# Optimization experiments

Hardware: AMD Instinct MI355X
Metric: run time of the kernel (lower is better)

Reference implementation:

```python
import jax, jax.numpy as jnp
import numpy as np

NHEADS = 16
HEAD_DIM = 128
HIDDEN = 2048
SOFTCAP = 50.0
ROPE_BASE = 10000.0
SCALE = 256.0 ** (-0.5)  # hardcoded in original, NOT head_dim**-0.5


def _rope_tables(T, D, dtype):
    inv_freq = 1.0 / (ROPE_BASE ** (jnp.arange(0, D, 2, dtype=jnp.float32) / D))
    pos = jnp.arange(T, dtype=jnp.float32)
    freqs = pos[:, None] * inv_freq[None, :]            # [T, D/2]
    emb = jnp.concatenate([freqs, freqs], axis=-1)      # [T, D]
    # broadcast shape [1, 1, T, D] for (B, H, T, D) q/k
    return jnp.cos(emb)[None, None].astype(dtype), jnp.sin(emb)[None, None].astype(dtype)


def _rotate_half(x):
    x1, x2 = x[..., : x.shape[-1] // 2], x[..., x.shape[-1] // 2:]
    return jnp.concatenate([-x2, x1], axis=-1)


def setup_inputs() -> dict:
    key = jax.random.key(0)
    ks = jax.random.split(key, 5)
    B, T = 1, 4096
    X = jax.random.normal(ks[0], (B, T, HIDDEN), dtype=jnp.float32)
    std = 0.02
    Wq = jax.random.normal(ks[1], (HIDDEN, NHEADS * HEAD_DIM), dtype=jnp.float32) * std
    Wk = jax.random.normal(ks[2], (HIDDEN, NHEADS * HEAD_DIM), dtype=jnp.float32) * std
    Wv = jax.random.normal(ks[3], (HIDDEN, NHEADS * HEAD_DIM), dtype=jnp.float32) * std
    Wo = jax.random.normal(ks[4], (NHEADS * HEAD_DIM, HIDDEN), dtype=jnp.float32) * std
    return {"X": X, "Wq": Wq, "Wk": Wk, "Wv": Wv, "Wo": Wo}


def reference(X, Wq, Wk, Wv, Wo):
    B, T, C = X.shape
    H, D = NHEADS, HEAD_DIM
    # QKV projections -> [B, H, T, D]
    q = (X @ Wq).reshape(B, T, H, D).transpose(0, 2, 1, 3)
    k = (X @ Wk).reshape(B, T, H, D).transpose(0, 2, 1, 3)
    v = (X @ Wv).reshape(B, T, H, D).transpose(0, 2, 1, 3)
    # RoPE
    cos, sin = _rope_tables(T, D, X.dtype)
    q = q * cos + _rotate_half(q) * sin
    k = k * cos + _rotate_half(k) * sin
    # attention logits with tanh softcapping
    att = jnp.einsum("bhqd,bhkd->bhqk", q, k) * SCALE
    att = jnp.tanh(att / SOFTCAP) * SOFTCAP
    causal = jnp.tril(jnp.ones((T, T), dtype=bool))[None, None]
    att = jnp.where(causal, att, -jnp.inf)
    att = jax.nn.softmax(att, axis=-1)
    # dropout is identity (train=False)
    y = jnp.einsum("bhqk,bhkd->bhqd", att, v)
    y = y.transpose(0, 2, 1, 3).reshape(B, T, H * D)
    return y @ Wo
```

## Files before the change

kernel.cpp:

```cpp
#include <hip/hip_runtime.h>
#include <stdint.h>

#define T_SEQ 4096
#define HID   2048
#define NH    16
#define HD    128

typedef __attribute__((ext_vector_type(8))) short short8;
typedef __attribute__((ext_vector_type(4))) short short4v;
typedef __attribute__((ext_vector_type(4))) float f32x4;

typedef __attribute__((address_space(1))) void as1_void;
typedef __attribute__((address_space(3))) void as3_void;

__device__ __forceinline__ unsigned short f2bf(float f){
  unsigned u = __builtin_bit_cast(unsigned, f);
  u += 0x7fffu + ((u >> 16) & 1u);
  return (unsigned short)(u >> 16);
}
__device__ __forceinline__ float bf2f(unsigned short b){
  unsigned u = ((unsigned)b) << 16;
  return __builtin_bit_cast(float, u);
}
__device__ __forceinline__ void gll16(const void* g, void* l){
  __builtin_amdgcn_global_load_lds((as1_void*)(uintptr_t)g,
                                   (as3_void*)(unsigned)(uintptr_t)l, 16, 0, 0);
}

__global__ __launch_bounds__(256) void conv_x_k(const float* __restrict__ X,
                                                unsigned short* __restrict__ O){
  int i = (blockIdx.x * 256 + threadIdx.x) * 4;
  float4 v = *(const float4*)(X + i);
  short4v o;
  o[0] = (short)f2bf(v.x); o[1] = (short)f2bf(v.y);
  o[2] = (short)f2bf(v.z); o[3] = (short)f2bf(v.w);
  *(short4v*)(O + i) = o;
}

__global__ __launch_bounds__(256) void conv_wt_k(const float* __restrict__ W0,
                                                 const float* __restrict__ W1,
                                                 const float* __restrict__ W2,
                                                 const float* __restrict__ W3,
                                                 unsigned short* __restrict__ Wt){
  const float* W = (blockIdx.z == 0) ? W0 : (blockIdx.z == 1) ? W1
                   : (blockIdx.z == 2) ? W2 : W3;
  unsigned short* out = Wt + (size_t)blockIdx.z * HID * HID;
  __shared__ float tile[32][33];
  const int x = threadIdx.x;
  const int y = threadIdx.y;
  const int k0 = blockIdx.y * 32, n0 = blockIdx.x * 32;
#pragma unroll
  for (int i = 0; i < 4; ++i){
    int r = y * 4 + i;
    tile[r][x] = W[(size_t)(k0 + r) * HID + n0 + x];
  }
  __syncthreads();
#pragma unroll
  for (int i = 0; i < 4; ++i){
    int r = y * 4 + i;
    out[(size_t)(n0 + r) * HID + k0 + x] = f2bf(tile[x][r]);
  }
}

template<int MODE, int NTOT>
__global__ __launch_bounds__(256, 3) void gemm_bt(
    const unsigned short* __restrict__ A,
    const unsigned short* __restrict__ Bt,
    unsigned short* __restrict__ Qb,
    unsigned short* __restrict__ Kb,
    unsigned short* __restrict__ Vt,
    float* __restrict__ Cf)
{
  constexpr int K = HID;
  __shared__ __align__(16) unsigned short lA[128 * 64];
  __shared__ __align__(16) unsigned short lB[128 * 64];

  const int tid  = threadIdx.x;
  const int wave = tid >> 6;
  const int lane = tid & 63;
  const int qd   = lane >> 4;
  const int mm   = lane & 15;
  const int m7   = mm & 7;
  const int wm   = wave >> 1;
  const int wn   = wave & 1;
  const int bm   = blockIdx.y * 128;
  const int bn   = blockIdx.x * 128;

  const unsigned short* ga[4];
  const unsigned short* gb[4];
  unsigned short* la[4];
  unsigned short* lbp[4];
#pragma unroll
  for (int i = 0; i < 4; ++i){
    int s0   = (wave * 4 + i) * 64;
    int slot = s0 + lane;
    int row  = slot >> 3;
    int kb   = (slot & 7) ^ (row & 7);
    ga[i]  = A  + (size_t)(bm + row) * K + kb * 8;
    gb[i]  = Bt + (size_t)(bn + row) * K + kb * 8;
    la[i]  = lA + s0 * 8;
    lbp[i] = lB + s0 * 8;
  }

  int abase[4], bbase[4];
#pragma unroll
  for (int t = 0; t < 4; ++t){
    abase[t] = (wm * 64 + t * 16 + mm) * 8;
    bbase[t] = (wn * 64 + t * 16 + mm) * 8;
  }

  const f32x4 fzero = {0.f, 0.f, 0.f, 0.f};
  f32x4 acc[4][4];
#pragma unroll
  for (int i = 0; i < 4; ++i)
#pragma unroll
    for (int j = 0; j < 4; ++j) acc[i][j] = fzero;

  for (int k0 = 0; k0 < K; k0 += 64){
    __syncthreads();
#pragma unroll
    for (int i = 0; i < 4; ++i){
      gll16(ga[i] + k0, la[i]);
      gll16(gb[i] + k0, lbp[i]);
    }
    __syncthreads();
#pragma unroll
    for (int ks = 0; ks < 2; ++ks){
      const int co = (ks * 4 + qd) ^ m7;
      short8 af[4], bfv[4];
#pragma unroll
      for (int t = 0; t < 4; ++t) af[t]  = *(const short8*)(lA + (abase[t] + co) * 8);
#pragma unroll
      for (int t = 0; t < 4; ++t) bfv[t] = *(const short8*)(lB + (bbase[t] + co) * 8);
#pragma unroll
      for (int i = 0; i < 4; ++i)
#pragma unroll
        for (int j = 0; j < 4; ++j)
          acc[i][j] = __builtin_amdgcn_mfma_f32_16x16x32_bf16(af[i], bfv[j], acc[i][j], 0, 0, 0);
    }
  }

#pragma unroll
  for (int i = 0; i < 4; ++i){
#pragma unroll
    for (int j = 0; j < 4; ++j){
      const int col = bn + wn * 64 + j * 16 + mm;
#pragma unroll
      for (int r = 0; r < 4; ++r){
        const int row = bm + wm * 64 + i * 16 + qd * 4 + r;
        const float v = acc[i][j][r];
        if (MODE == 0){
          const int sel = col >> 11;
          const int nn  = col & 2047;
          const int h   = nn >> 7;
          const int d   = nn & 127;
          const unsigned short bv = f2bf(v);
          if (sel == 0)      Qb[((size_t)h * T_SEQ + row) * HD + d] = bv;
          else if (sel == 1) Kb[((size_t)h * T_SEQ + row) * HD + d] = bv;
          else               Vt[((size_t)(h * HD + d)) * T_SEQ + row] = bv;
        } else {
          Cf[(size_t)row * NTOT + col] = v;
        }
      }
    }
  }
}

__global__ __launch_bounds__(256) void rope_k(unsigned short* __restrict__ Qb,
                                              unsigned short* __restrict__ Kb){
  const int j = threadIdx.x & 63;
  const int t = blockIdx.x * 4 + (threadIdx.x >> 6);
  const int h = blockIdx.y;
  const float fr = (float)t * __expf(-(float)j * (9.210340371976184f / 64.f));
  const float cs = cosf(fr), sn = sinf(fr);
  const size_t base = ((size_t)h * T_SEQ + t) * HD;
  {
    float x1 = bf2f(Qb[base + j]), x2 = bf2f(Qb[base + j + 64]);
    Qb[base + j]      = f2bf(x1 * cs - x2 * sn);
    Qb[base + j + 64] = f2bf(x2 * cs + x1 * sn);
  }
  {
    float x1 = bf2f(Kb[base + j]), x2 = bf2f(Kb[base + j + 64]);
    Kb[base + j]      = f2bf(x1 * cs - x2 * sn);
    Kb[base + j + 64] = f2bf(x2 * cs + x1 * sn);
  }
}

__global__ __launch_bounds__(256, 2) void attn_k(
    const unsigned short* __restrict__ Qb,
    const unsigned short* __restrict__ Kb,
    const unsigned short* __restrict__ Vt,
    unsigned short* __restrict__ Yb)
{
  __shared__ __align__(16) unsigned char smem[41216];
  unsigned short* lK = (unsigned short*)smem;
  unsigned short* lV = (unsigned short*)(smem + 16384);
  unsigned short (*lP)[32][32] = (unsigned short(*)[32][32])(smem + 32768);
  float* lL = (float*)(smem + 40960);
  float* lO = (float*)smem;

  const int tid  = threadIdx.x;
  const int w    = tid >> 6;
  const int rg   = w >> 1;
  const int kg   = w & 1;
  const int lane = tid & 63;
  const int qd   = lane >> 4;
  const int cc   = lane & 15;
  const int cx   = cc & 7;
  const int r8   = lane >> 3, c7 = lane & 7;

  const int b = blockIdx.x;
  const int h = (b & 7) + 8 * (b >> 8);
  const int pairP = (b >> 3) & 31;

  const int ce  = cc ^ qd;
  const int dlt = (ce & 4) ? -32 : 32;
  const unsigned short* gKbp = Kb + ((size_t)h * T_SEQ + w * 16 + qd) * HD + ce * 8;
  const int cV = c7 ^ r8;
  const unsigned short* gVbp = Vt + ((size_t)h * HD + w * 32 + r8) * T_SEQ + cV * 8;

  const f32x4 fzero = {0.f, 0.f, 0.f, 0.f};
  const float A0 = 0.0625f;
  const float A1 = -3.2552083e-8f;
  const float A2 = 2.0345052e-14f;

#pragma unroll 1
  for (int half = 0; half < 2; ++half){
    const int tp = half ? (63 - pairP) : pairP;
    const int qrow0 = tp * 64 + rg * 32;
    const int iters = tp + 1;

    short8 qf[2][4];
#pragma unroll
    for (int mt = 0; mt < 2; ++mt)
#pragma unroll
      for (int ks = 0; ks < 4; ++ks)
        qf[mt][ks] = *(const short8*)(Qb + ((size_t)h * T_SEQ + qrow0 + mt * 16 + cc) * HD + ks * 32 + qd * 8);

    f32x4 o[2][8];
    float lsum[2][4];
#pragma unroll
    for (int mt = 0; mt < 2; ++mt){
#pragma unroll
      for (int dn = 0; dn < 8; ++dn) o[mt][dn] = fzero;
#pragma unroll
      for (int r = 0; r < 4; ++r) lsum[mt][r] = 0.f;
    }

#pragma unroll 1
    for (int it = 0; it < iters; ++it){
      const int k0 = it * 64;
      __syncthreads();
      {
        const unsigned short* gK = gKbp + (size_t)k0 * HD;
        const unsigned short* gV = gVbp + k0;
        unsigned short* dK = lK + w * 2048;
        unsigned short* dV = lV + w * 2048;
#pragma unroll
        for (int i = 0; i < 4; ++i)
          gll16(gK + (size_t)(i * 4) * HD + ((i & 1) ? dlt : 0), dK + i * 512);
#pragma unroll
        for (int i = 0; i < 4; ++i)
          gll16(gV + (size_t)i * 8 * T_SEQ, dV + i * 512);
      }
      __syncthreads();

      f32x4 S[2][2];
#pragma unroll
      for (int mt = 0; mt < 2; ++mt)
#pragma unroll
        for (int nt = 0; nt < 2; ++nt) S[mt][nt] = fzero;
#pragma unroll
      for (int nt = 0; nt < 2; ++nt){
        short8 kf[4];
#pragma unroll
        for (int ks = 0; ks < 4; ++ks)
          kf[ks] = *(const short8*)(lK + ((kg * 32 + nt * 16 + cc) * 16 + ((ks * 4 + qd) ^ cx)) * 8);
#pragma unroll
        for (int mt = 0; mt < 2; ++mt)
#pragma unroll
          for (int ks = 0; ks < 4; ++ks)
            S[mt][nt] = __builtin_amdgcn_mfma_f32_16x16x32_bf16(qf[mt][ks], kf[ks], S[mt][nt], 0, 0, 0);
      }

      const bool domask = (it == iters - 1);
#pragma unroll
      for (int mt = 0; mt < 2; ++mt)
#pragma unroll
        for (int nt = 0; nt < 2; ++nt)
#pragma unroll
          for (int r = 0; r < 4; ++r){
            float s = S[mt][nt][r];
            float w2 = s * s;
            float t = fmaf(w2, A2, A1);
            t = fmaf(w2, t, A0);
            float a = s * t;
            a = fminf(fmaxf(a, -50.f), 50.f);
            float p = __expf(a);
            if (domask){
              int col = k0 + kg * 32 + nt * 16 + cc;
              int row = qrow0 + mt * 16 + qd * 4 + r;
              if (col > row) p = 0.f;
            }
            unsigned u = __builtin_bit_cast(unsigned, p);
            float pt = __builtin_bit_cast(float, u & 0xffff0000u);
            lsum[mt][r] += pt;
            lP[w][mt * 16 + qd * 4 + r][nt * 16 + cc] = (unsigned short)(u >> 16);
          }

      short8 pf[2];
#pragma unroll
      for (int mt = 0; mt < 2; ++mt)
        pf[mt] = *(const short8*)(&lP[w][mt * 16 + cc][qd * 8]);

#pragma unroll
      for (int dn = 0; dn < 8; ++dn){
        short8 vf = *(const short8*)(lV + ((dn * 16 + cc) * 8 + ((kg * 4 + qd) ^ cx)) * 8);
#pragma unroll
        for (int mt = 0; mt < 2; ++mt)
          o[mt][dn] = __builtin_amdgcn_mfma_f32_16x16x32_bf16(pf[mt], vf, o[mt][dn], 0, 0, 0);
      }
    }

    float lred[2][4];
#pragma unroll
    for (int mt = 0; mt < 2; ++mt)
#pragma unroll
      for (int r = 0; r < 4; ++r){
        float lb = lsum[mt][r];
        lb += __shfl_xor(lb, 1);
        lb += __shfl_xor(lb, 2);
        lb += __shfl_xor(lb, 4);
        lb += __shfl_xor(lb, 8);
        lred[mt][r] = lb;
      }

    __syncthreads();
    if (kg == 1){
#pragma unroll
      for (int mt = 0; mt < 2; ++mt){
#pragma unroll
        for (int dn = 0; dn < 8; ++dn)
          *(f32x4*)&lO[(dn * 16 + cc) * 68 + rg * 32 + mt * 16 + qd * 4] = o[mt][dn];
        if (cc == 0){
#pragma unroll
          for (int r = 0; r < 4; ++r)
            lL[rg * 32 + mt * 16 + qd * 4 + r] = lred[mt][r];
        }
      }
    }
    __syncthreads();
    if (kg == 0){
#pragma unroll
      for (int mt = 0; mt < 2; ++mt){
        float inv[4];
#pragma unroll
        for (int r = 0; r < 4; ++r){
          float lt = lred[mt][r] + lL[rg * 32 + mt * 16 + qd * 4 + r];
          inv[r] = __builtin_amdgcn_rcpf(lt);
        }
#pragma unroll
        for (int dn = 0; dn < 8; ++dn){
          f32x4 oo = o[mt][dn] + *(const f32x4*)&lO[(dn * 16 + cc) * 68 + rg * 32 + mt * 16 + qd * 4];
#pragma unroll
          for (int r = 0; r < 4; ++r){
            int row = qrow0 + mt * 16 + qd * 4 + r;
            Yb[(size_t)row * HID + h * HD + dn * 16 + cc] = f2bf(oo[r] * inv[r]);
          }
        }
      }
    }
    __syncthreads();
  }
}

extern "C" void kernel_launch(void* const* d_in, const int* in_sizes, int n_in,
                              void* d_out, int out_size, void* d_ws, size_t ws_size,
                              hipStream_t stream) {
  const float* X  = (const float*)d_in[0];
  const float* Wq = (const float*)d_in[1];
  const float* Wk = (const float*)d_in[2];
  const float* Wv = (const float*)d_in[3];
  const float* Wo = (const float*)d_in[4];
  float* out = (float*)d_out;

  unsigned short* ws = (unsigned short*)d_ws;
  unsigned short* Xb = ws;
  unsigned short* Wt = ws + (size_t)8  * 1024 * 1024;
  unsigned short* Qb = ws + (size_t)24 * 1024 * 1024;
  unsigned short* Kb = ws + (size_t)32 * 1024 * 1024;
  unsigned short* Vt = ws + (size_t)40 * 1024 * 1024;
  unsigned short* Yb = Xb;

  conv_x_k<<<8192, 256, 0, stream>>>(X, Xb);
  conv_wt_k<<<dim3(64, 64, 4), dim3(32, 8), 0, stream>>>(Wq, Wk, Wv, Wo, Wt);
  gemm_bt<0, 6144><<<dim3(48, 32), 256, 0, stream>>>(Xb, Wt, Qb, Kb, Vt, nullptr);
  rope_k<<<dim3(1024, NH), 256, 0, stream>>>(Qb, Kb);
  attn_k<<<dim3(512), 256, 0, stream>>>(Qb, Kb, Vt, Yb);
  gemm_bt<1, 2048><<<dim3(16, 32), 256, 0, stream>>>(Yb, Wt + (size_t)6144 * 2048,
                                                     nullptr, nullptr, nullptr, out);
}
```

Measured before the change: 432.4 us.

## Shrink attention LDS, one q-tile per block, raise occupancy to four blocks

The attention kernel now processes a single 64-row query tile per block instead of a paired short/long tile, launching 1024 blocks ordered longest-first. The P staging buffer now reuses the K tile region after an extra barrier, cutting LDS from about 41KB to 32KB, and launch bounds request four blocks per CU. The aim is better latency hiding and load balance through higher occupancy. The cost is an additional __syncthreads per iteration, register pressure from the tighter bound, and the loss of the paired-tile balancing.

```diff
diff --git a/kernel.cpp b/kernel.cpp
--- a/kernel.cpp
+++ b/kernel.cpp
@@ -186,17 +186,16 @@
   }
 }
 
-__global__ __launch_bounds__(256, 2) void attn_k(
+__global__ __launch_bounds__(256, 4) void attn_k(
     const unsigned short* __restrict__ Qb,
     const unsigned short* __restrict__ Kb,
     const unsigned short* __restrict__ Vt,
     unsigned short* __restrict__ Yb)
 {
-  __shared__ __align__(16) unsigned char smem[41216];
+  __shared__ __align__(16) unsigned char smem[32768];
   unsigned short* lK = (unsigned short*)smem;
   unsigned short* lV = (unsigned short*)(smem + 16384);
-  unsigned short (*lP)[32][32] = (unsigned short(*)[32][32])(smem + 32768);
-  float* lL = (float*)(smem + 40960);
+  float* lL = (float*)smem;
   float* lO = (float*)smem;
 
   const int tid  = threadIdx.x;
@@ -210,8 +209,8 @@
   const int r8   = lane >> 3, c7 = lane & 7;
 
   const int b = blockIdx.x;
-  const int h = (b & 7) + 8 * (b >> 8);
-  const int pairP = (b >> 3) & 31;
+  const int h = (b & 7) + 8 * ((b >> 3) & 1);
+  const int tp = 63 - (b >> 4);
 
   const int ce  = cc ^ qd;
   const int dlt = (ce & 4) ? -32 : 32;
@@ -219,158 +218,174 @@
   const int cV = c7 ^ r8;
   const unsigned short* gVbp = Vt + ((size_t)h * HD + w * 32 + r8) * T_SEQ + cV * 8;
 
+  unsigned short* lPw = lK + w * 2048;
+
   const f32x4 fzero = {0.f, 0.f, 0.f, 0.f};
   const float A0 = 0.0625f;
   const float A1 = -3.2552083e-8f;
   const float A2 = 2.0345052e-14f;
 
+  const int qrow0 = tp * 64 + rg * 32;
+  const int iters = tp + 1;
+
+  short8 qf[2][4];
+#pragma unroll
+  for (int mt = 0; mt < 2; ++mt)
+#pragma unroll
+    for (int ks = 0; ks < 4; ++ks)
+      qf[mt][ks] = *(const short8*)(Qb + ((size_t)h * T_SEQ + qrow0 + mt * 16 + cc) * HD + ks * 32 + qd * 8);
+
+  f32x4 o[2][8];
+  float lsum[2][4];
+#pragma unroll
+  for (int mt = 0; mt < 2; ++mt){
+#pragma unroll
+    for (int dn = 0; dn < 8; ++dn) o[mt][dn] = fzero;
+#pragma unroll
+    for (int r = 0; r < 4; ++r) lsum[mt][r] = 0.f;
+  }
+
 #pragma unroll 1
-  for (int half = 0; half < 2; ++half){
-    const int tp = half ? (63 - pairP) : pairP;
-    const int qrow0 = tp * 64 + rg * 32;
-    const int iters = tp + 1;
-
-    short8 qf[2][4];
-#pragma unroll
-    for (int mt = 0; mt < 2; ++mt)
+  for (int it = 0; it < iters; ++it){
+    const int k0 = it * 64;
+    __syncthreads();
+    {
+      const unsigned short* gK = gKbp + (size_t)k0 * HD;
+      const unsigned short* gV = gVbp + k0;
+      unsigned short* dK = lK + w * 2048;
+      unsigned short* dV = lV + w * 2048;
+#pragma unroll
+      for (int i = 0; i < 4; ++i)
+        gll16(gK + (size_t)(i * 4) * HD + ((i & 1) ? dlt : 0), dK + i * 512);
+#pragma unroll
+      for (int i = 0; i < 4; ++i)
+        gll16(gV + (size_t)i * 8 * T_SEQ, dV + i * 512);
+    }
+    __syncthreads();
+
+    f32x4 S[2][2];
+#pragma unroll
+    for (int mt = 0; mt < 2; ++mt)
+#pragma unroll
+      for (int nt = 0; nt < 2; ++nt) S[mt][nt] = fzero;
+#pragma unroll
+    for (int nt = 0; nt < 2; ++nt){
+      short8 kf[4];
 #pragma unroll
       for (int ks = 0; ks < 4; ++ks)
-        qf[mt][ks] = *(const short8*)(Qb + ((size_t)h * T_SEQ + qrow0 + mt * 16 + cc) * HD + ks * 32 + qd * 8);
-
-    f32x4 o[2][8];
-    float lsum[2][4];
+        kf[ks] = *(const short8*)(lK + ((kg * 32 + nt * 16 + cc) * 16 + ((ks * 4 + qd) ^ cx)) * 8);
+#pragma unroll
+      for (int mt = 0; mt < 2; ++mt)
+#pragma unroll
+        for (int ks = 0; ks < 4; ++ks)
+          S[mt][nt] = __builtin_amdgcn_mfma_f32_16x16x32_bf16(qf[mt][ks], kf[ks], S[mt][nt], 0, 0, 0);
+    }
+
+    const bool domask = (it == iters - 1);
+    unsigned short pv[2][2][4];
+#pragma unroll
+    for (int mt = 0; mt < 2; ++mt)
+#pragma unroll
+      for (int nt = 0; nt < 2; ++nt)
+#pragma unroll
+        for (int r = 0; r < 4; ++r){
+          float s = S[mt][nt][r];
+          float w2 = s * s;
+          float t = fmaf(w2, A2, A1);
+          t = fmaf(w2, t, A0);
+          float a = __builtin_amdgcn_fmed3f(s * t, -50.f, 50.f);
+          float p = __expf(a);
+          if (domask){
+            int col = k0 + kg * 32 + nt * 16 + cc;
+            int row = qrow0 + mt * 16 + qd * 4 + r;
+            if (col > row) p = 0.f;
+          }
+          unsigned u = __builtin_bit_cast(unsigned, p);
+          lsum[mt][r] += __builtin_bit_cast(float, u & 0xffff0000u);
+          pv[mt][nt][r] = (unsigned short)(u >> 16);
+        }
+
+    __syncthreads();
+
+#pragma unroll
+    for (int mt = 0; mt < 2; ++mt)
+#pragma unroll
+      for (int nt = 0; nt < 2; ++nt)
+#pragma unroll
+        for (int r = 0; r < 4; ++r)
+          lPw[(mt * 16 + qd * 4 + r) * 36 + nt * 16 + cc] = pv[mt][nt][r];
+
+    short8 pf[2];
 #pragma unroll
     for (int mt = 0; mt < 2; ++mt){
-#pragma unroll
-      for (int dn = 0; dn < 8; ++dn) o[mt][dn] = fzero;
-#pragma unroll
-      for (int r = 0; r < 4; ++r) lsum[mt][r] = 0.f;
-    }
-
-#pragma unroll 1
-    for (int it = 0; it < iters; ++it){
-      const int k0 = it * 64;
-      __syncthreads();
-      {
-        const unsigned short* gK = gKbp + (size_t)k0 * HD;
-        const unsigned short* gV = gVbp + k0;
-        unsigned short* dK = lK + w * 2048;
-        unsigned short* dV = lV + w * 2048;
-#pragma unroll
-        for (int i = 0; i < 4; ++i)
-          gll16(gK + (size_t)(i * 4) * HD + ((i & 1) ? dlt : 0), dK + i * 512);
-#pragma unroll
-        for (int i = 0; i < 4; ++i)
-          gll16(gV + (size_t)i * 8 * T_SEQ, dV + i * 512);
-      }
-      __syncthreads();
-
-      f32x4 S[2][2];
+      const unsigned short* pb = lPw + (mt * 16 + cc) * 36 + qd * 8;
+      union { short8 v; short4v hh[2]; } u;
+      u.hh[0] = *(const short4v*)pb;
+      u.hh[1] = *(const short4v*)(pb + 4);
+      pf[mt] = u.v;
+    }
+
+#pragma unroll
+    for (int dn = 0; dn < 8; ++dn){
+      short8 vf = *(const short8*)(lV + ((dn * 16 + cc) * 8 + ((kg * 4 + qd) ^ cx)) * 8);
 #pragma unroll
       for (int mt = 0; mt < 2; ++mt)
-#pragma unroll
-        for (int nt = 0; nt < 2; ++nt) S[mt][nt] = fzero;
-#pragma unroll
-      for (int nt = 0; nt < 2; ++nt){
-        short8 kf[4];
-#pragma unroll
-        for (int ks = 0; ks < 4; ++ks)
-          kf[ks] = *(const short8*)(lK + ((kg * 32 + nt * 16 + cc) * 16 + ((ks * 4 + qd) ^ cx)) * 8);
-#pragma unroll
-        for (int mt = 0; mt < 2; ++mt)
-#pragma unroll
-          for (int ks = 0; ks < 4; ++ks)
-            S[mt][nt] = __builtin_amdgcn_mfma_f32_16x16x32_bf16(qf[mt][ks], kf[ks], S[mt][nt], 0, 0, 0);
-      }
-
-      const bool domask = (it == iters - 1);
-#pragma unroll
-      for (int mt = 0; mt < 2; ++mt)
-#pragma unroll
-        for (int nt = 0; nt < 2; ++nt)
-#pragma unroll
-          for (int r = 0; r < 4; ++r){
-            float s = S[mt][nt][r];
-            float w2 = s * s;
-            float t = fmaf(w2, A2, A1);
-            t = fmaf(w2, t, A0);
-            float a = s * t;
-            a = fminf(fmaxf(a, -50.f), 50.f);
-            float p = __expf(a);
-            if (domask){
-              int col = k0 + kg * 32 + nt * 16 + cc;
-              int row = qrow0 + mt * 16 + qd * 4 + r;
-              if (col > row) p = 0.f;
-            }
-            unsigned u = __builtin_bit_cast(unsigned, p);
-            float pt = __builtin_bit_cast(float, u & 0xffff0000u);
-            lsum[mt][r] += pt;
-            lP[w][mt * 16 + qd * 4 + r][nt * 16 + cc] = (unsigned short)(u >> 16);
-          }
-
-      short8 pf[2];
-#pragma unroll
-      for (int mt = 0; mt < 2; ++mt)
-        pf[mt] = *(const short8*)(&lP[w][mt * 16 + cc][qd * 8]);
-
+        o[mt][dn] = __builtin_amdgcn_mfma_f32_16x16x32_bf16(pf[mt], vf, o[mt][dn], 0, 0, 0);
+    }
+  }
+
+  float lred[2][4];
+#pragma unroll
+  for (int mt = 0; mt < 2; ++mt)
+#pragma unroll
+    for (int r = 0; r < 4; ++r){
+      float lb = lsum[mt][r];
+      lb += __shfl_xor(lb, 1);
+      lb += __shfl_xor(lb, 2);
+      lb += __shfl_xor(lb, 4);
+      lb += __shfl_xor(lb, 8);
+      lred[mt][r] = lb;
+    }
+
+  __syncthreads();
+  if (kg == 1 && cc == 0){
+#pragma unroll
+    for (int mt = 0; mt < 2; ++mt)
+#pragma unroll
+      for (int r = 0; r < 4; ++r)
+        lL[rg * 32 + mt * 16 + qd * 4 + r] = lred[mt][r];
+  }
+  __syncthreads();
+  float inv[2][4];
+  if (kg == 0){
+#pragma unroll
+    for (int mt = 0; mt < 2; ++mt)
+#pragma unroll
+      for (int r = 0; r < 4; ++r)
+        inv[mt][r] = __builtin_amdgcn_rcpf(lred[mt][r] + lL[rg * 32 + mt * 16 + qd * 4 + r]);
+  }
+  __syncthreads();
+  if (kg == 1){
+#pragma unroll
+    for (int mt = 0; mt < 2; ++mt)
+#pragma unroll
+      for (int dn = 0; dn < 8; ++dn)
+        *(f32x4*)&lO[(dn * 16 + cc) * 64 + rg * 32 + mt * 16 + qd * 4] = o[mt][dn];
+  }
+  __syncthreads();
+  if (kg == 0){
+#pragma unroll
+    for (int mt = 0; mt < 2; ++mt){
 #pragma unroll
       for (int dn = 0; dn < 8; ++dn){
-        short8 vf = *(const short8*)(lV + ((dn * 16 + cc) * 8 + ((kg * 4 + qd) ^ cx)) * 8);
-#pragma unroll
-        for (int mt = 0; mt < 2; ++mt)
-          o[mt][dn] = __builtin_amdgcn_mfma_f32_16x16x32_bf16(pf[mt], vf, o[mt][dn], 0, 0, 0);
-      }
-    }
-
-    float lred[2][4];
-#pragma unroll
-    for (int mt = 0; mt < 2; ++mt)
-#pragma unroll
-      for (int r = 0; r < 4; ++r){
-        float lb = lsum[mt][r];
-        lb += __shfl_xor(lb, 1);
-        lb += __shfl_xor(lb, 2);
-        lb += __shfl_xor(lb, 4);
-        lb += __shfl_xor(lb, 8);
-        lred[mt][r] = lb;
-      }
-
-    __syncthreads();
-    if (kg == 1){
-#pragma unroll
-      for (int mt = 0; mt < 2; ++mt){
-#pragma unroll
-        for (int dn = 0; dn < 8; ++dn)
-          *(f32x4*)&lO[(dn * 16 + cc) * 68 + rg * 32 + mt * 16 + qd * 4] = o[mt][dn];
-        if (cc == 0){
-#pragma unroll
-          for (int r = 0; r < 4; ++r)
-            lL[rg * 32 + mt * 16 + qd * 4 + r] = lred[mt][r];
+        f32x4 oo = o[mt][dn] + *(const f32x4*)&lO[(dn * 16 + cc) * 64 + rg * 32 + mt * 16 + qd * 4];
+#pragma unroll
+        for (int r = 0; r < 4; ++r){
+          int row = qrow0 + mt * 16 + qd * 4 + r;
+          Yb[(size_t)row * HID + h * HD + dn * 16 + cc] = f2bf(oo[r] * inv[mt][r]);
         }
       }
     }
-    __syncthreads();
-    if (kg == 0){
-#pragma unroll
-      for (int mt = 0; mt < 2; ++mt){
-        float inv[4];
-#pragma unroll
-        for (int r = 0; r < 4; ++r){
-          float lt = lred[mt][r] + lL[rg * 32 + mt * 16 + qd * 4 + r];
-          inv[r] = __builtin_amdgcn_rcpf(lt);
-        }
-#pragma unroll
-        for (int dn = 0; dn < 8; ++dn){
-          f32x4 oo = o[mt][dn] + *(const f32x4*)&lO[(dn * 16 + cc) * 68 + rg * 32 + mt * 16 + qd * 4];
-#pragma unroll
-          for (int r = 0; r < 4; ++r){
-            int row = qrow0 + mt * 16 + qd * 4 + r;
-            Yb[(size_t)row * HID + h * HD + dn * 16 + cc] = f2bf(oo[r] * inv[r]);
-          }
-        }
-      }
-    }
-    __syncthreads();
   }
 }
 
@@ -396,7 +411,7 @@
   conv_wt_k<<<dim3(64, 64, 4), dim3(32, 8), 0, stream>>>(Wq, Wk, Wv, Wo, Wt);
   gemm_bt<0, 6144><<<dim3(48, 32), 256, 0, stream>>>(Xb, Wt, Qb, Kb, Vt, nullptr);
   rope_k<<<dim3(1024, NH), 256, 0, stream>>>(Qb, Kb);
-  attn_k<<<dim3(512), 256, 0, stream>>>(Qb, Kb, Vt, Yb);
+  attn_k<<<dim3(1024), 256, 0, stream>>>(Qb, Kb, Vt, Yb);
   gemm_bt<1, 2048><<<dim3(16, 32), 256, 0, stream>>>(Yb, Wt + (size_t)6144 * 2048,
                                                      nullptr, nullptr, nullptr, out);
 }
```

New measurement: 616.8 us. 42.6% more time.
